# Optimization experiments

Measured on AMD Instinct MI355X. Metric: run time of the kernel, lower is better.

Reference implementation:

```python
import math
import jax, jax.numpy as jnp
import numpy as np

SDE_THRESHOLD = 10.0
ANGLE_THRESHOLD_DEG = 30.0


def setup_inputs() -> dict:
    key = jax.random.key(0)
    k1, k2 = jax.random.split(key)
    B, H, N = 8, 16, 1024
    y_pred = jax.random.normal(k1, (B, H, 4), dtype=jnp.float32)
    sample_points = jax.random.normal(k2, (B, N, 3), dtype=jnp.float32)
    return {"y_pred": y_pred, "sample_points": sample_points}


def reference(y_pred, sample_points):
    # y_pred: [B,H,4] = (nx,ny,nz,d) per plane head; sample_points: [B,N,3]
    B, H, _ = y_pred.shape
    n = y_pred[..., :3]
    n = n / jnp.linalg.norm(n, axis=-1, keepdims=True)  # normalize normals
    d = y_pred[..., 3]

    # transform_representation_cm: represent plane by (normal, point) where
    # point = projection of the point-cloud centroid onto the plane n.x + d = 0
    cm = sample_points.mean(axis=1)  # [B,3]
    point = cm[:, None, :] - (jnp.einsum('bhd,bd->bh', n, cm) + d)[..., None] * n  # [B,H,3]

    # chamfer_adapter: reflect points across each plane, bidirectional chamfer (squared dists)
    proj = jnp.einsum('bnd,bhd->bhn', sample_points, n) + d[:, :, None]  # [B,H,N]
    refl = sample_points[:, None, :, :] - 2.0 * proj[..., None] * n[:, :, None, :]  # [B,H,N,3]
    rr = jnp.sum(refl * refl, axis=-1)                  # [B,H,N]
    ss = jnp.sum(sample_points * sample_points, axis=-1)  # [B,N]
    cross = jnp.einsum('bhid,bjd->bhij', refl, sample_points)  # [B,H,N,N]
    d2 = rr[..., None] + ss[:, None, None, :] - 2.0 * cross
    sde = jnp.min(d2, axis=-1).mean(axis=-1) + jnp.min(d2, axis=-2).mean(axis=-1)  # [B,H]

    # minmax_normalization -> confidence = 1 - (sde - min) / |max - min| per batch row
    mn = sde.min(axis=1, keepdims=True)
    mx = sde.max(axis=1, keepdims=True)
    conf = 1.0 - (sde - mn) / jnp.abs(mx - mn)

    # pairwise angle-based duplicate suppression (vectorized NMS)
    cos = jnp.clip(jnp.einsum('bhd,bgd->bhg', n, n), -1.0, 1.0)
    ang = jnp.arccos(cos) * (180.0 / math.pi)
    close = (ang < ANGLE_THRESHOLD_DEG) | (180.0 - ang < ANGLE_THRESHOLD_DEG)
    close = close & ~jnp.eye(H, dtype=bool)
    valid = sde <= SDE_THRESHOLD  # filter x.sde <= sde_threshold
    # plane i is popped iff exists valid j (close) with sde_i >= sde_j (equal sde pops both)
    sup = valid & jnp.any(close & valid[:, None, :] & (sde[:, :, None] >= sde[:, None, :]), axis=-1)
    keep = valid & ~sup

    # to_tensor(): [normal(3), point(3), confidence, sde]; sort kept by confidence desc,
    # zero-pad suppressed/filtered slots (fixed shape [B,H,8] instead of ragged pad_sequence)
    planes = jnp.concatenate([n, point, conf[..., None], sde[..., None]], axis=-1)  # [B,H,8]
    sort_key = jnp.where(keep, conf, -jnp.inf)
    order = jnp.argsort(-sort_key, axis=1)
    planes_s = jnp.take_along_axis(planes, order[..., None], axis=1)
    keep_s = jnp.take_along_axis(keep, order, axis=1)
    return jnp.where(keep_s[..., None], planes_s, 0.0)
```

## Files before the change

### kernel.cpp

```cpp
#include <hip/hip_runtime.h>
#include <math.h>

#define BB 8
#define HH 16
#define NN 1024
#define TB 256
#define NSC 4
#define SCH 256
#define POWN 4
#define SUMBASE (BB * HH * NSC * NN)


__global__ __launch_bounds__(TB) void chamfer_kernel(
    const float* __restrict__ y_pred,
    const float* __restrict__ sp,
    float* __restrict__ ws)
{
    __shared__ __align__(16) float4 pts[SCH];

    const int blk = blockIdx.x;
    const int bh  = blk >> 2;
    const int sc  = blk & (NSC - 1);
    const int b   = bh >> 4;
    const int tid = threadIdx.x;

    float pnx = y_pred[bh * 4 + 0];
    float pny = y_pred[bh * 4 + 1];
    float pnz = y_pred[bh * 4 + 2];
    float pd  = y_pred[bh * 4 + 3];
    float inv = 1.0f / sqrtf(pnx * pnx + pny * pny + pnz * pnz);
    pnx *= inv; pny *= inv; pnz *= inv;

    const float* __restrict__ spb = sp + (size_t)b * NN * 3;

    {
        int j = sc * SCH + tid;
        float x = spb[j * 3 + 0], y = spb[j * 3 + 1], z = spb[j * 3 + 2];
        pts[tid] = make_float4(x, y, z, x * x + y * y + z * z);
    }

    float mx[POWN], my[POWN], mz[POWN], osq[POWN];
#pragma unroll
    for (int u = 0; u < POWN; ++u) {
        int i = u * TB + tid;
        float x = spb[i * 3 + 0], y = spb[i * 3 + 1], z = spb[i * 3 + 2];
        float proj = x * pnx + y * pny + z * pnz + pd;
        x -= 2.0f * proj * pnx;
        y -= 2.0f * proj * pny;
        z -= 2.0f * proj * pnz;
        osq[u] = x * x + y * y + z * z;
        mx[u] = -2.0f * x; my[u] = -2.0f * y; mz[u] = -2.0f * z;
    }
    __syncthreads();

    float m0[POWN], m1[POWN];
#pragma unroll
    for (int u = 0; u < POWN; ++u) { m0[u] = 3.4e38f; m1[u] = 3.4e38f; }

#define DIST(qq, u) fmaf(mx[u], qq.x, fmaf(my[u], qq.y, fmaf(mz[u], qq.z, qq.w)))
    for (int j = 0; j < SCH; j += 4) {
        float4 q0 = pts[j + 0];
        float4 q1 = pts[j + 1];
        float4 q2 = pts[j + 2];
        float4 q3 = pts[j + 3];
#pragma unroll
        for (int u = 0; u < POWN; ++u) {
            float d0 = DIST(q0, u);
            float d1 = DIST(q1, u);
            float d2 = DIST(q2, u);
            float d3 = DIST(q3, u);
            m0[u] = fminf(fminf(m0[u], d0), d1);
            m1[u] = fminf(fminf(m1[u], d2), d3);
        }
    }
#undef DIST

    float* wp = ws + (size_t)(bh * NSC + sc) * NN;
#pragma unroll
    for (int u = 0; u < POWN; ++u)
        wp[u * TB + tid] = osq[u] + fminf(m0[u], m1[u]);
}

__global__ __launch_bounds__(TB) void reduce_kernel(
    const float* __restrict__ ws_in,
    float* __restrict__ ws_out)
{
    __shared__ float wsum[4];
    const int bh  = blockIdx.x;
    const int tid = threadIdx.x;

    const float4* r0 = (const float4*)(ws_in + (size_t)(bh * NSC + 0) * NN);
    const float4* r1 = (const float4*)(ws_in + (size_t)(bh * NSC + 1) * NN);
    const float4* r2 = (const float4*)(ws_in + (size_t)(bh * NSC + 2) * NN);
    const float4* r3 = (const float4*)(ws_in + (size_t)(bh * NSC + 3) * NN);

    float4 a0 = r0[tid], a1 = r1[tid], a2 = r2[tid], a3 = r3[tid];
    float e0 = fminf(fminf(a0.x, a1.x), fminf(a2.x, a3.x));
    float e1 = fminf(fminf(a0.y, a1.y), fminf(a2.y, a3.y));
    float e2 = fminf(fminf(a0.z, a1.z), fminf(a2.z, a3.z));
    float e3 = fminf(fminf(a0.w, a1.w), fminf(a2.w, a3.w));
    float s  = (e0 + e1) + (e2 + e3);

    for (int off = 32; off; off >>= 1) s += __shfl_down(s, off, 64);
    if ((tid & 63) == 0) wsum[tid >> 6] = s;
    __syncthreads();
    if (tid == 0)
        ws_out[SUMBASE + bh] = (wsum[0] + wsum[1]) + (wsum[2] + wsum[3]);
}

__global__ __launch_bounds__(TB) void finalize_kernel(
    const float* __restrict__ ws,
    const float* __restrict__ y_pred,
    const float* __restrict__ sp,
    float* __restrict__ out)
{
    const int b   = blockIdx.x;
    const int tid = threadIdx.x;

    __shared__ float sde_s[HH], nx_s[HH], ny_s[HH], nz_s[HH], d_s[HH], conf_s[HH];
    __shared__ float cmacc[3];
    __shared__ int keep_s[HH];

    if (tid < 3) cmacc[tid] = 0.0f;
    __syncthreads();

    const float* spb = sp + (size_t)b * NN * 3;
    float sx = 0.0f, sy = 0.0f, sz = 0.0f;
    for (int p = tid; p < NN; p += TB) {
        sx += spb[p * 3 + 0];
        sy += spb[p * 3 + 1];
        sz += spb[p * 3 + 2];
    }
    for (int off = 32; off; off >>= 1) {
        sx += __shfl_down(sx, off, 64);
        sy += __shfl_down(sy, off, 64);
        sz += __shfl_down(sz, off, 64);
    }
    if ((tid & 63) == 0) {
        atomicAdd(&cmacc[0], sx);
        atomicAdd(&cmacc[1], sy);
        atomicAdd(&cmacc[2], sz);
    }
    __syncthreads();

    const float cmx = cmacc[0] / NN, cmy = cmacc[1] / NN, cmz = cmacc[2] / NN;

    if (tid < HH) {
        int h = tid;
        float nx = y_pred[(b * HH + h) * 4 + 0];
        float ny = y_pred[(b * HH + h) * 4 + 1];
        float nz = y_pred[(b * HH + h) * 4 + 2];
        float d  = y_pred[(b * HH + h) * 4 + 3];
        float inv = 1.0f / sqrtf(nx * nx + ny * ny + nz * nz);
        nx *= inv; ny *= inv; nz *= inv;
        nx_s[h] = nx; ny_s[h] = ny; nz_s[h] = nz; d_s[h] = d;
        sde_s[h] = ws[SUMBASE + b * HH + h] * (2.0f / NN);
    }
    __syncthreads();

    if (tid < HH) {
        int h = tid;
        float mn = sde_s[0], mx = sde_s[0];
        for (int g = 1; g < HH; ++g) {
            mn = fminf(mn, sde_s[g]);
            mx = fmaxf(mx, sde_s[g]);
        }
        float sde  = sde_s[h];
        float conf = 1.0f - (sde - mn) / fabsf(mx - mn);
        conf_s[h]  = conf;
        bool valid = (sde <= 10.0f);
        bool sup   = false;
        if (valid) {
            for (int g = 0; g < HH; ++g) {
                if (g == h) continue;
                float c = nx_s[h] * nx_s[g] + ny_s[h] * ny_s[g] + nz_s[h] * nz_s[g];
                c = fminf(1.0f, fmaxf(-1.0f, c));
                float ang = acosf(c) * 57.29577951308232f;
                bool close = (ang < 30.0f) || (180.0f - ang < 30.0f);
                if (close && (sde_s[g] <= 10.0f) && (sde >= sde_s[g])) sup = true;
            }
        }
        keep_s[h] = (valid && !sup) ? 1 : 0;
    }
    __syncthreads();

    if (tid < HH) {
        int h = tid;
        float keyh = keep_s[h] ? conf_s[h] : -INFINITY;
        int pos = 0;
        for (int g = 0; g < HH; ++g) {
            float keyg = keep_s[g] ? conf_s[g] : -INFINITY;
            if (keyg > keyh || (keyg == keyh && g < h)) ++pos;
        }
        float nx = nx_s[h], ny = ny_s[h], nz = nz_s[h];
        float t  = nx * cmx + ny * cmy + nz * cmz + d_s[h];
        float px = cmx - t * nx, py = cmy - t * ny, pz = cmz - t * nz;

        float* o = out + (size_t)(b * HH + pos) * 8;
        if (keep_s[h]) {
            o[0] = nx; o[1] = ny; o[2] = nz;
            o[3] = px; o[4] = py; o[5] = pz;
            o[6] = conf_s[h];
            o[7] = sde_s[h];
        } else {
            for (int c = 0; c < 8; ++c) o[c] = 0.0f;
        }
    }
}

extern "C" void kernel_launch(void* const* d_in, const int* in_sizes, int n_in,
                              void* d_out, int out_size, void* d_ws, size_t ws_size,
                              hipStream_t stream) {
    const float* y_pred = (const float*)d_in[0];
    const float* sp     = (const float*)d_in[1];
    float* out          = (float*)d_out;
    float* ws           = (float*)d_ws;

    chamfer_kernel<<<dim3(BB * HH * NSC), dim3(TB), 0, stream>>>(y_pred, sp, ws);
    reduce_kernel<<<dim3(BB * HH), dim3(TB), 0, stream>>>(ws, ws);
    finalize_kernel<<<dim3(BB), dim3(TB), 0, stream>>>(ws, y_pred, sp, out);
}
```

Baseline: 75.40 us.

## Fuse chunk min-reduction into finalize and split chamfer into more smaller blocks

```diff
diff --git a/kernel.cpp b/kernel.cpp
--- a/kernel.cpp
+++ b/kernel.cpp
@@ -4,14 +4,14 @@
 #define BB 8
 #define HH 16
 #define NN 1024
-#define TB 256
-#define NSC 4
-#define SCH 256
-#define POWN 4
-#define SUMBASE (BB * HH * NSC * NN)
-
-
-__global__ __launch_bounds__(TB) void chamfer_kernel(
+#define TBC 128
+#define NSC 8
+#define SCH 128
+#define POWN 8
+#define TBF 1024
+
+
+__global__ __launch_bounds__(TBC) void chamfer_kernel(
     const float* __restrict__ y_pred,
     const float* __restrict__ sp,
     float* __restrict__ ws)
@@ -19,7 +19,7 @@
     __shared__ __align__(16) float4 pts[SCH];
 
     const int blk = blockIdx.x;
-    const int bh  = blk >> 2;
+    const int bh  = blk >> 3;
     const int sc  = blk & (NSC - 1);
     const int b   = bh >> 4;
     const int tid = threadIdx.x;
@@ -42,7 +42,7 @@
     float mx[POWN], my[POWN], mz[POWN], osq[POWN];
 #pragma unroll
     for (int u = 0; u < POWN; ++u) {
-        int i = u * TB + tid;
+        int i = u * TBC + tid;
         float x = spb[i * 3 + 0], y = spb[i * 3 + 1], z = spb[i * 3 + 2];
         float proj = x * pnx + y * pny + z * pnz + pd;
         x -= 2.0f * proj * pnx;
@@ -78,37 +78,10 @@
     float* wp = ws + (size_t)(bh * NSC + sc) * NN;
 #pragma unroll
     for (int u = 0; u < POWN; ++u)
-        wp[u * TB + tid] = osq[u] + fminf(m0[u], m1[u]);
+        wp[u * TBC + tid] = osq[u] + fminf(m0[u], m1[u]);
 }
 
-__global__ __launch_bounds__(TB) void reduce_kernel(
-    const float* __restrict__ ws_in,
-    float* __restrict__ ws_out)
-{
-    __shared__ float wsum[4];
-    const int bh  = blockIdx.x;
-    const int tid = threadIdx.x;
-
-    const float4* r0 = (const float4*)(ws_in + (size_t)(bh * NSC + 0) * NN);
-    const float4* r1 = (const float4*)(ws_in + (size_t)(bh * NSC + 1) * NN);
-    const float4* r2 = (const float4*)(ws_in + (size_t)(bh * NSC + 2) * NN);
-    const float4* r3 = (const float4*)(ws_in + (size_t)(bh * NSC + 3) * NN);
-
-    float4 a0 = r0[tid], a1 = r1[tid], a2 = r2[tid], a3 = r3[tid];
-    float e0 = fminf(fminf(a0.x, a1.x), fminf(a2.x, a3.x));
-    float e1 = fminf(fminf(a0.y, a1.y), fminf(a2.y, a3.y));
-    float e2 = fminf(fminf(a0.z, a1.z), fminf(a2.z, a3.z));
-    float e3 = fminf(fminf(a0.w, a1.w), fminf(a2.w, a3.w));
-    float s  = (e0 + e1) + (e2 + e3);
-
-    for (int off = 32; off; off >>= 1) s += __shfl_down(s, off, 64);
-    if ((tid & 63) == 0) wsum[tid >> 6] = s;
-    __syncthreads();
-    if (tid == 0)
-        ws_out[SUMBASE + bh] = (wsum[0] + wsum[1]) + (wsum[2] + wsum[3]);
-}
-
-__global__ __launch_bounds__(TB) void finalize_kernel(
+__global__ __launch_bounds__(TBF) void finalize_kernel(
     const float* __restrict__ ws,
     const float* __restrict__ y_pred,
     const float* __restrict__ sp,
@@ -116,35 +89,65 @@
 {
     const int b   = blockIdx.x;
     const int tid = threadIdx.x;
+    const int w   = tid >> 6;
+    const int ln  = tid & 63;
 
     __shared__ float sde_s[HH], nx_s[HH], ny_s[HH], nz_s[HH], d_s[HH], conf_s[HH];
-    __shared__ float cmacc[3];
+    __shared__ float wred[16][3];
+    __shared__ float cms[3];
     __shared__ int keep_s[HH];
 
-    if (tid < 3) cmacc[tid] = 0.0f;
-    __syncthreads();
-
     const float* spb = sp + (size_t)b * NN * 3;
-    float sx = 0.0f, sy = 0.0f, sz = 0.0f;
-    for (int p = tid; p < NN; p += TB) {
-        sx += spb[p * 3 + 0];
-        sy += spb[p * 3 + 1];
-        sz += spb[p * 3 + 2];
-    }
-    for (int off = 32; off; off >>= 1) {
-        sx += __shfl_down(sx, off, 64);
-        sy += __shfl_down(sy, off, 64);
-        sz += __shfl_down(sz, off, 64);
-    }
-    if ((tid & 63) == 0) {
-        atomicAdd(&cmacc[0], sx);
-        atomicAdd(&cmacc[1], sy);
-        atomicAdd(&cmacc[2], sz);
-    }
-    __syncthreads();
-
-    const float cmx = cmacc[0] / NN, cmy = cmacc[1] / NN, cmz = cmacc[2] / NN;
-
+    {
+        float sx = spb[tid * 3 + 0];
+        float sy = spb[tid * 3 + 1];
+        float sz = spb[tid * 3 + 2];
+        for (int off = 32; off; off >>= 1) {
+            sx += __shfl_down(sx, off, 64);
+            sy += __shfl_down(sy, off, 64);
+            sz += __shfl_down(sz, off, 64);
+        }
+        if (ln == 0) { wred[w][0] = sx; wred[w][1] = sy; wred[w][2] = sz; }
+    }
+
+    {
+        const int h = w;
+        const float* base = ws + (size_t)((b * HH + h) * NSC) * NN;
+        const float4* r0 = (const float4*)(base + 0 * NN);
+        const float4* r1 = (const float4*)(base + 1 * NN);
+        const float4* r2 = (const float4*)(base + 2 * NN);
+        const float4* r3 = (const float4*)(base + 3 * NN);
+        const float4* r4 = (const float4*)(base + 4 * NN);
+        const float4* r5 = (const float4*)(base + 5 * NN);
+        const float4* r6 = (const float4*)(base + 6 * NN);
+        const float4* r7 = (const float4*)(base + 7 * NN);
+        float acc = 0.0f;
+        for (int k = 0; k < 4; ++k) {
+            int i4 = ln + 64 * k;
+            float4 a0 = r0[i4], a1 = r1[i4], a2 = r2[i4], a3 = r3[i4];
+            float4 a4 = r4[i4], a5 = r5[i4], a6 = r6[i4], a7 = r7[i4];
+            float e0 = fminf(fminf(fminf(a0.x, a1.x), fminf(a2.x, a3.x)),
+                             fminf(fminf(a4.x, a5.x), fminf(a6.x, a7.x)));
+            float e1 = fminf(fminf(fminf(a0.y, a1.y), fminf(a2.y, a3.y)),
+                             fminf(fminf(a4.y, a5.y), fminf(a6.y, a7.y)));
+            float e2 = fminf(fminf(fminf(a0.z, a1.z), fminf(a2.z, a3.z)),
+                             fminf(fminf(a4.z, a5.z), fminf(a6.z, a7.z)));
+            float e3 = fminf(fminf(fminf(a0.w, a1.w), fminf(a2.w, a3.w)),
+                             fminf(fminf(a4.w, a5.w), fminf(a6.w, a7.w)));
+            acc += (e0 + e1) + (e2 + e3);
+        }
+        for (int off = 32; off; off >>= 1) acc += __shfl_down(acc, off, 64);
+        if (ln == 0) sde_s[h] = acc;
+    }
+    __syncthreads();
+
+    if (tid == 0) {
+        float X = 0.0f, Y = 0.0f, Z = 0.0f;
+        for (int g = 0; g < 16; ++g) {
+            X += wred[g][0]; Y += wred[g][1]; Z += wred[g][2];
+        }
+        cms[0] = X / NN; cms[1] = Y / NN; cms[2] = Z / NN;
+    }
     if (tid < HH) {
         int h = tid;
         float nx = y_pred[(b * HH + h) * 4 + 0];
@@ -154,7 +157,7 @@
         float inv = 1.0f / sqrtf(nx * nx + ny * ny + nz * nz);
         nx *= inv; ny *= inv; nz *= inv;
         nx_s[h] = nx; ny_s[h] = ny; nz_s[h] = nz; d_s[h] = d;
-        sde_s[h] = ws[SUMBASE + b * HH + h] * (2.0f / NN);
+        sde_s[h] = sde_s[h] * (2.0f / NN);
     }
     __syncthreads();
 
@@ -192,6 +195,7 @@
             float keyg = keep_s[g] ? conf_s[g] : -INFINITY;
             if (keyg > keyh || (keyg == keyh && g < h)) ++pos;
         }
+        float cmx = cms[0], cmy = cms[1], cmz = cms[2];
         float nx = nx_s[h], ny = ny_s[h], nz = nz_s[h];
         float t  = nx * cmx + ny * cmy + nz * cmz + d_s[h];
         float px = cmx - t * nx, py = cmy - t * ny, pz = cmz - t * nz;
@@ -216,7 +220,6 @@
     float* out          = (float*)d_out;
     float* ws           = (float*)d_ws;
 
-    chamfer_kernel<<<dim3(BB * HH * NSC), dim3(TB), 0, stream>>>(y_pred, sp, ws);
-    reduce_kernel<<<dim3(BB * HH), dim3(TB), 0, stream>>>(ws, ws);
-    finalize_kernel<<<dim3(BB), dim3(TB), 0, stream>>>(ws, y_pred, sp, out);
+    chamfer_kernel<<<dim3(BB * HH * NSC), dim3(TBC), 0, stream>>>(y_pred, sp, ws);
+    finalize_kernel<<<dim3(BB), dim3(TBF), 0, stream>>>(ws, y_pred, sp, out);
 }
```

Result: slower. 79.35 us (+5.2%).

## Fuse chamfer, reduce and finalize kernels via last-block atomic counters

Applied to the files above, without the earlier changes.

```diff
diff --git a/kernel.cpp b/kernel.cpp
--- a/kernel.cpp
+++ b/kernel.cpp
@@ -11,12 +11,21 @@
 #define SUMBASE (BB * HH * NSC * NN)
 
 
-__global__ __launch_bounds__(TB) void chamfer_kernel(
+__device__ int g_cnt_bh[BB * HH];
+__device__ int g_cnt_b[BB];
+
+__global__ __launch_bounds__(TB) void fused_kernel(
     const float* __restrict__ y_pred,
     const float* __restrict__ sp,
-    float* __restrict__ ws)
+    float* __restrict__ ws,
+    float* __restrict__ out)
 {
     __shared__ __align__(16) float4 pts[SCH];
+    __shared__ float wsum[4];
+    __shared__ int s_last;
+    __shared__ float sde_s[HH], nx_s[HH], ny_s[HH], nz_s[HH], d_s[HH], conf_s[HH];
+    __shared__ float cmacc[3];
+    __shared__ int keep_s[HH];
 
     const int blk = blockIdx.x;
     const int bh  = blk >> 2;
@@ -24,122 +33,129 @@
     const int b   = bh >> 4;
     const int tid = threadIdx.x;
 
-    float pnx = y_pred[bh * 4 + 0];
-    float pny = y_pred[bh * 4 + 1];
-    float pnz = y_pred[bh * 4 + 2];
-    float pd  = y_pred[bh * 4 + 3];
-    float inv = 1.0f / sqrtf(pnx * pnx + pny * pny + pnz * pnz);
-    pnx *= inv; pny *= inv; pnz *= inv;
-
-    const float* __restrict__ spb = sp + (size_t)b * NN * 3;
-
     {
-        int j = sc * SCH + tid;
-        float x = spb[j * 3 + 0], y = spb[j * 3 + 1], z = spb[j * 3 + 2];
-        pts[tid] = make_float4(x, y, z, x * x + y * y + z * z);
-    }
-
-    float mx[POWN], my[POWN], mz[POWN], osq[POWN];
-#pragma unroll
-    for (int u = 0; u < POWN; ++u) {
-        int i = u * TB + tid;
-        float x = spb[i * 3 + 0], y = spb[i * 3 + 1], z = spb[i * 3 + 2];
-        float proj = x * pnx + y * pny + z * pnz + pd;
-        x -= 2.0f * proj * pnx;
-        y -= 2.0f * proj * pny;
-        z -= 2.0f * proj * pnz;
-        osq[u] = x * x + y * y + z * z;
-        mx[u] = -2.0f * x; my[u] = -2.0f * y; mz[u] = -2.0f * z;
-    }
-    __syncthreads();
-
-    float m0[POWN], m1[POWN];
-#pragma unroll
-    for (int u = 0; u < POWN; ++u) { m0[u] = 3.4e38f; m1[u] = 3.4e38f; }
+        float pnx = y_pred[bh * 4 + 0];
+        float pny = y_pred[bh * 4 + 1];
+        float pnz = y_pred[bh * 4 + 2];
+        float pd  = y_pred[bh * 4 + 3];
+        float inv = 1.0f / sqrtf(pnx * pnx + pny * pny + pnz * pnz);
+        pnx *= inv; pny *= inv; pnz *= inv;
+
+        const float* __restrict__ spb = sp + (size_t)b * NN * 3;
+
+        {
+            int j = sc * SCH + tid;
+            float x = spb[j * 3 + 0], y = spb[j * 3 + 1], z = spb[j * 3 + 2];
+            pts[tid] = make_float4(x, y, z, x * x + y * y + z * z);
+        }
+
+        float mx[POWN], my[POWN], mz[POWN], osq[POWN];
+#pragma unroll
+        for (int u = 0; u < POWN; ++u) {
+            int i = u * TB + tid;
+            float x = spb[i * 3 + 0], y = spb[i * 3 + 1], z = spb[i * 3 + 2];
+            float proj = x * pnx + y * pny + z * pnz + pd;
+            x -= 2.0f * proj * pnx;
+            y -= 2.0f * proj * pny;
+            z -= 2.0f * proj * pnz;
+            osq[u] = x * x + y * y + z * z;
+            mx[u] = -2.0f * x; my[u] = -2.0f * y; mz[u] = -2.0f * z;
+        }
+        __syncthreads();
+
+        float m0[POWN], m1[POWN];
+#pragma unroll
+        for (int u = 0; u < POWN; ++u) { m0[u] = 3.4e38f; m1[u] = 3.4e38f; }
 
 #define DIST(qq, u) fmaf(mx[u], qq.x, fmaf(my[u], qq.y, fmaf(mz[u], qq.z, qq.w)))
-    for (int j = 0; j < SCH; j += 4) {
-        float4 q0 = pts[j + 0];
-        float4 q1 = pts[j + 1];
-        float4 q2 = pts[j + 2];
-        float4 q3 = pts[j + 3];
-#pragma unroll
-        for (int u = 0; u < POWN; ++u) {
-            float d0 = DIST(q0, u);
-            float d1 = DIST(q1, u);
-            float d2 = DIST(q2, u);
-            float d3 = DIST(q3, u);
-            m0[u] = fminf(fminf(m0[u], d0), d1);
-            m1[u] = fminf(fminf(m1[u], d2), d3);
-        }
-    }
+        for (int j = 0; j < SCH; j += 4) {
+            float4 q0 = pts[j + 0];
+            float4 q1 = pts[j + 1];
+            float4 q2 = pts[j + 2];
+            float4 q3 = pts[j + 3];
+#pragma unroll
+            for (int u = 0; u < POWN; ++u) {
+                float d0 = DIST(q0, u);
+                float d1 = DIST(q1, u);
+                float d2 = DIST(q2, u);
+                float d3 = DIST(q3, u);
+                m0[u] = fminf(fminf(m0[u], d0), d1);
+                m1[u] = fminf(fminf(m1[u], d2), d3);
+            }
+        }
 #undef DIST
 
-    float* wp = ws + (size_t)(bh * NSC + sc) * NN;
-#pragma unroll
-    for (int u = 0; u < POWN; ++u)
-        wp[u * TB + tid] = osq[u] + fminf(m0[u], m1[u]);
-}
-
-__global__ __launch_bounds__(TB) void reduce_kernel(
-    const float* __restrict__ ws_in,
-    float* __restrict__ ws_out)
-{
-    __shared__ float wsum[4];
-    const int bh  = blockIdx.x;
-    const int tid = threadIdx.x;
-
-    const float4* r0 = (const float4*)(ws_in + (size_t)(bh * NSC + 0) * NN);
-    const float4* r1 = (const float4*)(ws_in + (size_t)(bh * NSC + 1) * NN);
-    const float4* r2 = (const float4*)(ws_in + (size_t)(bh * NSC + 2) * NN);
-    const float4* r3 = (const float4*)(ws_in + (size_t)(bh * NSC + 3) * NN);
-
-    float4 a0 = r0[tid], a1 = r1[tid], a2 = r2[tid], a3 = r3[tid];
-    float e0 = fminf(fminf(a0.x, a1.x), fminf(a2.x, a3.x));
-    float e1 = fminf(fminf(a0.y, a1.y), fminf(a2.y, a3.y));
-    float e2 = fminf(fminf(a0.z, a1.z), fminf(a2.z, a3.z));
-    float e3 = fminf(fminf(a0.w, a1.w), fminf(a2.w, a3.w));
-    float s  = (e0 + e1) + (e2 + e3);
-
-    for (int off = 32; off; off >>= 1) s += __shfl_down(s, off, 64);
-    if ((tid & 63) == 0) wsum[tid >> 6] = s;
-    __syncthreads();
-    if (tid == 0)
-        ws_out[SUMBASE + bh] = (wsum[0] + wsum[1]) + (wsum[2] + wsum[3]);
-}
-
-__global__ __launch_bounds__(TB) void finalize_kernel(
-    const float* __restrict__ ws,
-    const float* __restrict__ y_pred,
-    const float* __restrict__ sp,
-    float* __restrict__ out)
-{
-    const int b   = blockIdx.x;
-    const int tid = threadIdx.x;
-
-    __shared__ float sde_s[HH], nx_s[HH], ny_s[HH], nz_s[HH], d_s[HH], conf_s[HH];
-    __shared__ float cmacc[3];
-    __shared__ int keep_s[HH];
+        float* wp = ws + (size_t)(bh * NSC + sc) * NN;
+#pragma unroll
+        for (int u = 0; u < POWN; ++u)
+            wp[u * TB + tid] = osq[u] + fminf(m0[u], m1[u]);
+    }
+
+    __threadfence();
+    __syncthreads();
+    if (tid == 0) {
+        int t = atomicAdd(&g_cnt_bh[bh], 1);
+        s_last = (t == NSC - 1) ? 1 : 0;
+    }
+    __syncthreads();
+    if (!s_last) return;
+
+    __threadfence();
+    {
+        const float* base = ws + (size_t)(bh * NSC) * NN;
+        const float4* r0 = (const float4*)(base + 0 * NN);
+        const float4* r1 = (const float4*)(base + 1 * NN);
+        const float4* r2 = (const float4*)(base + 2 * NN);
+        const float4* r3 = (const float4*)(base + 3 * NN);
+
+        float4 a0 = r0[tid], a1 = r1[tid], a2 = r2[tid], a3 = r3[tid];
+        float e0 = fminf(fminf(a0.x, a1.x), fminf(a2.x, a3.x));
+        float e1 = fminf(fminf(a0.y, a1.y), fminf(a2.y, a3.y));
+        float e2 = fminf(fminf(a0.z, a1.z), fminf(a2.z, a3.z));
+        float e3 = fminf(fminf(a0.w, a1.w), fminf(a2.w, a3.w));
+        float s  = (e0 + e1) + (e2 + e3);
+
+        for (int off = 32; off; off >>= 1) s += __shfl_down(s, off, 64);
+        if ((tid & 63) == 0) wsum[tid >> 6] = s;
+        __syncthreads();
+        if (tid == 0)
+            ws[SUMBASE + bh] = (wsum[0] + wsum[1]) + (wsum[2] + wsum[3]);
+    }
+
+    __threadfence();
+    __syncthreads();
+    if (tid == 0) {
+        atomicExch(&g_cnt_bh[bh], 0);
+        int t = atomicAdd(&g_cnt_b[b], 1);
+        s_last = (t == HH - 1) ? 1 : 0;
+    }
+    __syncthreads();
+    if (!s_last) return;
+
+    __threadfence();
+    if (tid == 0) atomicExch(&g_cnt_b[b], 0);
 
     if (tid < 3) cmacc[tid] = 0.0f;
     __syncthreads();
 
     const float* spb = sp + (size_t)b * NN * 3;
-    float sx = 0.0f, sy = 0.0f, sz = 0.0f;
-    for (int p = tid; p < NN; p += TB) {
-        sx += spb[p * 3 + 0];
-        sy += spb[p * 3 + 1];
-        sz += spb[p * 3 + 2];
-    }
-    for (int off = 32; off; off >>= 1) {
-        sx += __shfl_down(sx, off, 64);
-        sy += __shfl_down(sy, off, 64);
-        sz += __shfl_down(sz, off, 64);
-    }
-    if ((tid & 63) == 0) {
-        atomicAdd(&cmacc[0], sx);
-        atomicAdd(&cmacc[1], sy);
-        atomicAdd(&cmacc[2], sz);
+    {
+        float sx = 0.0f, sy = 0.0f, sz = 0.0f;
+        for (int p = tid; p < NN; p += TB) {
+            sx += spb[p * 3 + 0];
+            sy += spb[p * 3 + 1];
+            sz += spb[p * 3 + 2];
+        }
+        for (int off = 32; off; off >>= 1) {
+            sx += __shfl_down(sx, off, 64);
+            sy += __shfl_down(sy, off, 64);
+            sz += __shfl_down(sz, off, 64);
+        }
+        if ((tid & 63) == 0) {
+            atomicAdd(&cmacc[0], sx);
+            atomicAdd(&cmacc[1], sy);
+            atomicAdd(&cmacc[2], sz);
+        }
     }
     __syncthreads();
 
@@ -216,7 +232,5 @@
     float* out          = (float*)d_out;
     float* ws           = (float*)d_ws;
 
-    chamfer_kernel<<<dim3(BB * HH * NSC), dim3(TB), 0, stream>>>(y_pred, sp, ws);
-    reduce_kernel<<<dim3(BB * HH), dim3(TB), 0, stream>>>(ws, ws);
-    finalize_kernel<<<dim3(BB), dim3(TB), 0, stream>>>(ws, y_pred, sp, out);
+    fused_kernel<<<dim3(BB * HH * NSC), dim3(TB), 0, stream>>>(y_pred, sp, ws, out);
 }
```

After: 185.9 us. 147% more time.
